# Kernel tuning notes

Measured on AMD Instinct MI355X. Metric: run time of the kernel, lower is better.

Reference implementation:

```python
import jax, jax.numpy as jnp
import numpy as np

EPS = 1e-8  # torch F.cosine_similarity eps


def setup_inputs() -> dict:
    key = jax.random.key(0)
    ks = jax.random.split(key, 12)
    B, H, W, D, Tq = 16, 32, 32, 768, 1024
    s = 1.0 / np.sqrt(D)
    inp = {
        "image_features": jax.random.normal(ks[0], (B, H, W, D), jnp.float32),
        "text_features": jax.random.normal(ks[1], (B, Tq, D), jnp.float32),
        "image_padding_mask": jax.random.randint(ks[2], (B, H, W), 0, 2).astype(bool),
        "Wq": jax.random.normal(ks[3], (D, D), jnp.float32) * s,
        "bq": jnp.zeros((D,), jnp.float32),
        "Wk": jax.random.normal(ks[4], (D, D), jnp.float32) * s,
        "bk": jnp.zeros((D,), jnp.float32),
        "W1": jax.random.normal(ks[5], (16, 1), jnp.float32),
        "b1": jnp.zeros((16,), jnp.float32),
        "W2": jax.random.normal(ks[6], (1, 16), jnp.float32) * 0.25,
        "b2": jnp.zeros((1,), jnp.float32),
    }
    return inp


def reference(image_features, text_features, image_padding_mask,
              Wq, bq, Wk, bk, W1, b1, W2, b2):
    B, H, W_, D = image_features.shape
    # projections (torch Linear: x @ W.T + b)
    q = text_features @ Wq.T + bq                      # [B, Tq, D]
    k = (image_features @ Wk.T + bk).reshape(B, H * W_, D)  # [B, Tk, D]
    pad = image_padding_mask.reshape(B, H * W_)        # [B, Tk] True = pad
    # cosine similarity: normalize with eps-clamped norms, then dot
    qn = q / jnp.maximum(jnp.linalg.norm(q, axis=-1, keepdims=True), EPS)
    kn = k / jnp.maximum(jnp.linalg.norm(k, axis=-1, keepdims=True), EPS)
    scores = jnp.einsum('bqd,bkd->bqk', qn, kn)        # [B, Tq, Tk]
    scores = jnp.where(pad[:, None, :], -jnp.inf, scores)
    max_w = scores.max(axis=-1)                        # [B, Tq]
    # tiny MLP 1 -> 16 -> 1 with sigmoid
    h = jax.nn.relu(max_w[..., None] @ W1.T + b1)      # [B, Tq, 16]
    out = jax.nn.sigmoid(h @ W2.T + b2)[..., 0]        # [B, Tq]
    return out
```

## Files before the change

kernel.cpp:

```cpp
#include <hip/hip_runtime.h>
#include <math.h>

typedef float  f32x4 __attribute__((ext_vector_type(4)));
typedef short  s16x8 __attribute__((ext_vector_type(8)));
typedef unsigned short u16x4 __attribute__((ext_vector_type(4)));
typedef unsigned short u16x8 __attribute__((ext_vector_type(8)));

__device__ __forceinline__ unsigned short f2bf(float f) {
  unsigned u = __float_as_uint(f);
  u += 0x7FFFu + ((u >> 16) & 1u);
  return (unsigned short)(u >> 16);
}
__device__ __forceinline__ float bf2f(unsigned short h) {
  return __uint_as_float(((unsigned)h) << 16);
}
__device__ __forceinline__ unsigned fenc(float f) {
  unsigned u = __float_as_uint(f);
  return (u & 0x80000000u) ? ~u : (u | 0x80000000u);
}
__device__ __forceinline__ float fdec(unsigned u) {
  u = (u & 0x80000000u) ? (u & 0x7FFFFFFFu) : ~u;
  return __uint_as_float(u);
}
__device__ __forceinline__ void gload16(const void* g, void* l) {
  __builtin_amdgcn_global_load_lds(
      (const __attribute__((address_space(1))) unsigned int*)g,
      (__attribute__((address_space(3))) unsigned int*)l, 16, 0, 0);
}

__global__ __launch_bounds__(256) void init_bufs(unsigned* __restrict__ um,
                                                 float* __restrict__ qs,
                                                 float* __restrict__ ks, int n) {
  int i = blockIdx.x * 256 + threadIdx.x;
  if (i < n) { um[i] = 0x007FFFFFu; qs[i] = 0.f; ks[i] = 0.f; }
}

__global__ __launch_bounds__(256) void cvt2(const float* __restrict__ a,
                                            const float* __restrict__ b,
                                            unsigned short* __restrict__ da,
                                            unsigned short* __restrict__ db, int n4) {
  int i = blockIdx.x * 256 + threadIdx.x;
  int stride = gridDim.x * 256;
  for (; i < 2 * n4; i += stride) {
    const float* s = (i < n4) ? a : b;
    unsigned short* d = (i < n4) ? da : db;
    int j = (i < n4) ? i : i - n4;
    f32x4 v = ((const f32x4*)s)[j];
    u16x4 o;
    o[0] = f2bf(v[0]); o[1] = f2bf(v[1]); o[2] = f2bf(v[2]); o[3] = f2bf(v[3]);
    ((u16x4*)d)[j] = o;
  }
}

__global__ __launch_bounds__(256) void proj(const float* __restrict__ Xq,
                                            const float* __restrict__ Xk,
                                            const unsigned short* __restrict__ Wqb,
                                            const unsigned short* __restrict__ Wkb,
                                            const float* __restrict__ bq,
                                            const float* __restrict__ bk,
                                            unsigned short* __restrict__ Qh,
                                            unsigned short* __restrict__ Kh,
                                            float* __restrict__ qssq,
                                            float* __restrict__ kssq) {
  const int K = 768;
  __shared__ __align__(16) unsigned short sA[128 * 64];
  __shared__ __align__(16) unsigned short sB[128 * 64];
  int id = blockIdx.x;
  int xcd = id & 7, j = id >> 3;
  int by = j % 6, bxl = j / 6;
  int bx = xcd * 16 + bxl;
  const float* A; const unsigned short* Bw; const float* bias;
  unsigned short* Out; float* ssq;
  if (blockIdx.z == 0) { A = Xq; Bw = Wqb; bias = bq; Out = Qh; ssq = qssq; }
  else                 { A = Xk; Bw = Wkb; bias = bk; Out = Kh; ssq = kssq; }

  const int t = threadIdx.x;
  const int lane = t & 63, w = t >> 6;
  const int wr = w >> 1, wc = w & 1;
  const int m0 = bx * 128, n0 = by * 128;
  const float* Ab = A + (size_t)m0 * K;
  const unsigned short* Bb = Bw + (size_t)n0 * K;
  f32x4 acc[4][4] = {};
  const int srow = t >> 3;
  const int scol = (t & 7) * 8;
  const int hsw = scol ^ ((srow & 7) << 3);
  const int lg = lane >> 4, li = lane & 15;

  for (int k0 = 0; k0 < K; k0 += 64) {
#pragma unroll
    for (int s = 0; s < 4; ++s) {
      int row = srow + s * 32;
      gload16(Bb + (size_t)row * K + k0 + hsw, (char*)sB + t * 16 + s * 4096);
    }
#pragma unroll
    for (int s = 0; s < 4; ++s) {
      int row = srow + s * 32;
      const float* src = Ab + (size_t)row * K + k0 + scol;
      f32x4 v0 = *(const f32x4*)(src);
      f32x4 v1 = *(const f32x4*)(src + 4);
      u16x8 o;
      o[0] = f2bf(v0[0]); o[1] = f2bf(v0[1]); o[2] = f2bf(v0[2]); o[3] = f2bf(v0[3]);
      o[4] = f2bf(v1[0]); o[5] = f2bf(v1[1]); o[6] = f2bf(v1[2]); o[7] = f2bf(v1[3]);
      *(u16x8*)(sA + row * 64 + (scol ^ ((row & 7) << 3))) = o;
    }
    __syncthreads();
#pragma unroll
    for (int ks = 0; ks < 2; ++ks) {
      s16x8 af[4], bfr[4];
#pragma unroll
      for (int mi = 0; mi < 4; ++mi) {
        int row = wr * 64 + mi * 16 + li;
        af[mi] = *(const s16x8*)(sA + row * 64 + ((ks * 32 + lg * 8) ^ ((row & 7) << 3)));
      }
#pragma unroll
      for (int ni = 0; ni < 4; ++ni) {
        int row = wc * 64 + ni * 16 + li;
        bfr[ni] = *(const s16x8*)(sB + row * 64 + ((ks * 32 + lg * 8) ^ ((row & 7) << 3)));
      }
#pragma unroll
      for (int mi = 0; mi < 4; ++mi)
#pragma unroll
        for (int ni = 0; ni < 4; ++ni)
          acc[mi][ni] = __builtin_amdgcn_mfma_f32_16x16x32_bf16(af[mi], bfr[ni], acc[mi][ni], 0, 0, 0);
    }
    __syncthreads();
  }
  float bv[4]; int col[4];
#pragma unroll
  for (int ni = 0; ni < 4; ++ni) { col[ni] = n0 + wc * 64 + ni * 16 + li; bv[ni] = bias[col[ni]]; }
#pragma unroll
  for (int mi = 0; mi < 4; ++mi) {
    int rbase = m0 + wr * 64 + mi * 16 + lg * 4;
#pragma unroll
    for (int r = 0; r < 4; ++r) {
      float s = 0.f;
#pragma unroll
      for (int ni = 0; ni < 4; ++ni) {
        float v = acc[mi][ni][r] + bv[ni];
        Out[(size_t)(rbase + r) * 768 + col[ni]] = f2bf(v);
        s += v * v;
      }
#pragma unroll
      for (int off = 1; off < 16; off <<= 1) s += __shfl_xor(s, off, 64);
      if (li == 0) atomicAdd(&ssq[rbase + r], s);
    }
  }
}

__global__ __launch_bounds__(256) void scores_max(const unsigned short* __restrict__ Qh,
                                                  const unsigned short* __restrict__ Kh,
                                                  const float* __restrict__ kssq,
                                                  const int* __restrict__ pad,
                                                  unsigned* __restrict__ umax) {
  const int K = 768;
  __shared__ __align__(16) unsigned short sA[128 * 64];
  __shared__ __align__(16) unsigned short sB[128 * 64];
  int id = blockIdx.x;
  int x = id & 7, g = id >> 3;
  int tile = g & 63;
  int qt = tile & 7, kt = tile >> 3;
  int b = ((g >> 6) << 3) | x;

  const int t = threadIdx.x;
  const int lane = t & 63, w = t >> 6;
  const int wr = w >> 1, wc = w & 1;
  const unsigned short* Ab = Qh + ((size_t)b * 1024 + qt * 128) * K;
  const unsigned short* Bb = Kh + ((size_t)b * 1024 + kt * 128) * K;
  f32x4 acc[4][4] = {};
  const int srow = t >> 3;
  const int scol = (t & 7) * 8;
  const int hsw = scol ^ ((srow & 7) << 3);
  const int lg = lane >> 4, li = lane & 15;

  for (int k0 = 0; k0 < K; k0 += 64) {
#pragma unroll
    for (int s = 0; s < 4; ++s) {
      int row = srow + s * 32;
      gload16(Ab + (size_t)row * K + k0 + hsw, (char*)sA + t * 16 + s * 4096);
      gload16(Bb + (size_t)row * K + k0 + hsw, (char*)sB + t * 16 + s * 4096);
    }
    __syncthreads();
#pragma unroll
    for (int ks = 0; ks < 2; ++ks) {
      s16x8 af[4], bfr[4];
#pragma unroll
      for (int mi = 0; mi < 4; ++mi) {
        int row = wr * 64 + mi * 16 + li;
        af[mi] = *(const s16x8*)(sA + row * 64 + ((ks * 32 + lg * 8) ^ ((row & 7) << 3)));
      }
#pragma unroll
      for (int ni = 0; ni < 4; ++ni) {
        int row = wc * 64 + ni * 16 + li;
        bfr[ni] = *(const s16x8*)(sB + row * 64 + ((ks * 32 + lg * 8) ^ ((row & 7) << 3)));
      }
#pragma unroll
      for (int mi = 0; mi < 4; ++mi)
#pragma unroll
        for (int ni = 0; ni < 4; ++ni)
          acc[mi][ni] = __builtin_amdgcn_mfma_f32_16x16x32_bf16(af[mi], bfr[ni], acc[mi][ni], 0, 0, 0);
    }
    __syncthreads();
  }
  float rk[4]; bool valid[4];
#pragma unroll
  for (int ni = 0; ni < 4; ++ni) {
    int gcol = b * 1024 + kt * 128 + wc * 64 + ni * 16 + li;
    rk[ni] = 1.0f / fmaxf(sqrtf(kssq[gcol]), 1e-8f);
    valid[ni] = (pad[gcol] == 0);
  }
#pragma unroll
  for (int mi = 0; mi < 4; ++mi) {
#pragma unroll
    for (int r = 0; r < 4; ++r) {
      float v = -INFINITY;
#pragma unroll
      for (int ni = 0; ni < 4; ++ni)
        if (valid[ni]) v = fmaxf(v, acc[mi][ni][r] * rk[ni]);
#pragma unroll
      for (int off = 1; off < 16; off <<= 1) v = fmaxf(v, __shfl_xor(v, off, 64));
      if (li == 0) {
        int row = b * 1024 + qt * 128 + wr * 64 + mi * 16 + lg * 4 + r;
        atomicMax(&umax[row], fenc(v));
      }
    }
  }
}

__global__ __launch_bounds__(256) void mlp_kernel(const unsigned* __restrict__ umax,
                                                  const float* __restrict__ qssq,
                                                  const float* __restrict__ w1,
                                                  const float* __restrict__ b1,
                                                  const float* __restrict__ w2,
                                                  const float* __restrict__ b2,
                                                  float* __restrict__ out, int n) {
  int i = blockIdx.x * 256 + threadIdx.x;
  if (i >= n) return;
  float m = fdec(umax[i]) / fmaxf(sqrtf(qssq[i]), 1e-8f);
  float s = b2[0];
#pragma unroll
  for (int j = 0; j < 16; ++j) s += w2[j] * fmaxf(m * w1[j] + b1[j], 0.f);
  out[i] = 1.f / (1.f + expf(-s));
}

extern "C" void kernel_launch(void* const* d_in, const int* in_sizes, int n_in,
                              void* d_out, int out_size, void* d_ws, size_t ws_size,
                              hipStream_t stream) {
  const float* image = (const float*)d_in[0];
  const float* text  = (const float*)d_in[1];
  const int*   pad   = (const int*)d_in[2];
  const float* Wq    = (const float*)d_in[3];
  const float* bq    = (const float*)d_in[4];
  const float* Wk    = (const float*)d_in[5];
  const float* bk    = (const float*)d_in[6];
  const float* W1    = (const float*)d_in[7];
  const float* b1    = (const float*)d_in[8];
  const float* W2    = (const float*)d_in[9];
  const float* b2    = (const float*)d_in[10];
  float* out = (float*)d_out;

  char* ws = (char*)d_ws;
  unsigned short* Qh  = (unsigned short*)(ws);
  unsigned short* Kh  = (unsigned short*)(ws + 25165824);
  unsigned short* Wqb = (unsigned short*)(ws + 50331648);
  unsigned short* Wkb = (unsigned short*)(ws + 51511296);
  unsigned*       um  = (unsigned*)(ws + 52690944);
  float*          qss = (float*)(ws + 52756480);
  float*          kss = (float*)(ws + 52822016);

  init_bufs<<<64, 256, 0, stream>>>(um, qss, kss, 16384);
  cvt2<<<1152, 256, 0, stream>>>(Wq, Wk, Wqb, Wkb, 147456);
  proj<<<dim3(768, 1, 2), 256, 0, stream>>>(text, image, Wqb, Wkb, bq, bk, Qh, Kh, qss, kss);
  scores_max<<<1024, 256, 0, stream>>>(Qh, Kh, kss, pad, um);
  mlp_kernel<<<64, 256, 0, stream>>>(um, qss, W1, b1, W2, b2, out, 16384);
}
```

Before: 243.7 us.

## Double-buffer LDS in both GEMMs and fuse MLP epilogue via tile ticket counter

Both the projection GEMM and the scores GEMM now use two LDS buffers, prefetching the next K-slice while MFMAs run on the current one, which removes one barrier per iteration. The init kernel is replaced by a memset, using a shifted max encoding so that zero is the identity. The separate MLP kernel is folded into scores_max: the last block to finish each query tile (found with an atomic ticket counter) applies the MLP. This cuts two launches and hides load latency, at the cost of doubled LDS (64KB per block), which may lower occupancy.

```diff
diff --git a/kernel.cpp b/kernel.cpp
--- a/kernel.cpp
+++ b/kernel.cpp
@@ -11,14 +11,13 @@
   u += 0x7FFFu + ((u >> 16) & 1u);
   return (unsigned short)(u >> 16);
 }
-__device__ __forceinline__ float bf2f(unsigned short h) {
-  return __uint_as_float(((unsigned)h) << 16);
-}
-__device__ __forceinline__ unsigned fenc(float f) {
+__device__ __forceinline__ unsigned fenc2(float f) {
   unsigned u = __float_as_uint(f);
-  return (u & 0x80000000u) ? ~u : (u | 0x80000000u);
-}
-__device__ __forceinline__ float fdec(unsigned u) {
+  u = (u & 0x80000000u) ? ~u : (u | 0x80000000u);
+  return u - 0x007FFFFFu;
+}
+__device__ __forceinline__ float fdec2(unsigned u) {
+  u += 0x007FFFFFu;
   u = (u & 0x80000000u) ? (u & 0x7FFFFFFFu) : ~u;
   return __uint_as_float(u);
 }
@@ -26,13 +25,6 @@
   __builtin_amdgcn_global_load_lds(
       (const __attribute__((address_space(1))) unsigned int*)g,
       (__attribute__((address_space(3))) unsigned int*)l, 16, 0, 0);
-}
-
-__global__ __launch_bounds__(256) void init_bufs(unsigned* __restrict__ um,
-                                                 float* __restrict__ qs,
-                                                 float* __restrict__ ks, int n) {
-  int i = blockIdx.x * 256 + threadIdx.x;
-  if (i < n) { um[i] = 0x007FFFFFu; qs[i] = 0.f; ks[i] = 0.f; }
 }
 
 __global__ __launch_bounds__(256) void cvt2(const float* __restrict__ a,
@@ -63,8 +55,8 @@
                                             float* __restrict__ qssq,
                                             float* __restrict__ kssq) {
   const int K = 768;
-  __shared__ __align__(16) unsigned short sA[128 * 64];
-  __shared__ __align__(16) unsigned short sB[128 * 64];
+  __shared__ __align__(16) unsigned short sA[2][128 * 64];
+  __shared__ __align__(16) unsigned short sB[2][128 * 64];
   int id = blockIdx.x;
   int xcd = id & 7, j = id >> 3;
   int by = j % 6, bxl = j / 6;
@@ -86,42 +78,76 @@
   const int hsw = scol ^ ((srow & 7) << 3);
   const int lg = lane >> 4, li = lane & 15;
 
-  for (int k0 = 0; k0 < K; k0 += 64) {
+#pragma unroll
+  for (int s = 0; s < 4; ++s) {
+    int row = srow + s * 32;
+    gload16(Bb + (size_t)row * K + hsw, (char*)sB[0] + t * 16 + s * 4096);
+  }
+  {
+    f32x4 v0[4], v1[4];
+#pragma unroll
+    for (int s = 0; s < 4; ++s) {
+      const float* src = Ab + (size_t)(srow + s * 32) * K + scol;
+      v0[s] = *(const f32x4*)src; v1[s] = *(const f32x4*)(src + 4);
+    }
 #pragma unroll
     for (int s = 0; s < 4; ++s) {
       int row = srow + s * 32;
-      gload16(Bb + (size_t)row * K + k0 + hsw, (char*)sB + t * 16 + s * 4096);
-    }
-#pragma unroll
-    for (int s = 0; s < 4; ++s) {
-      int row = srow + s * 32;
-      const float* src = Ab + (size_t)row * K + k0 + scol;
-      f32x4 v0 = *(const f32x4*)(src);
-      f32x4 v1 = *(const f32x4*)(src + 4);
       u16x8 o;
-      o[0] = f2bf(v0[0]); o[1] = f2bf(v0[1]); o[2] = f2bf(v0[2]); o[3] = f2bf(v0[3]);
-      o[4] = f2bf(v1[0]); o[5] = f2bf(v1[1]); o[6] = f2bf(v1[2]); o[7] = f2bf(v1[3]);
-      *(u16x8*)(sA + row * 64 + (scol ^ ((row & 7) << 3))) = o;
-    }
-    __syncthreads();
+      o[0] = f2bf(v0[s][0]); o[1] = f2bf(v0[s][1]); o[2] = f2bf(v0[s][2]); o[3] = f2bf(v0[s][3]);
+      o[4] = f2bf(v1[s][0]); o[5] = f2bf(v1[s][1]); o[6] = f2bf(v1[s][2]); o[7] = f2bf(v1[s][3]);
+      *(u16x8*)(sA[0] + row * 64 + (scol ^ ((row & 7) << 3))) = o;
+    }
+  }
+  __syncthreads();
+
+  for (int kt = 0; kt < 12; ++kt) {
+    const int cur = kt & 1;
+    const unsigned short* cA = sA[cur];
+    const unsigned short* cB = sB[cur];
+    f32x4 p0[4], p1[4];
+    const bool pre = (kt < 11);
+    if (pre) {
+      const int k0n = (kt + 1) * 64;
+#pragma unroll
+      for (int s = 0; s < 4; ++s) {
+        int row = srow + s * 32;
+        gload16(Bb + (size_t)row * K + k0n + hsw, (char*)sB[cur ^ 1] + t * 16 + s * 4096);
+      }
+#pragma unroll
+      for (int s = 0; s < 4; ++s) {
+        const float* src = Ab + (size_t)(srow + s * 32) * K + k0n + scol;
+        p0[s] = *(const f32x4*)src; p1[s] = *(const f32x4*)(src + 4);
+      }
+    }
 #pragma unroll
     for (int ks = 0; ks < 2; ++ks) {
       s16x8 af[4], bfr[4];
 #pragma unroll
       for (int mi = 0; mi < 4; ++mi) {
         int row = wr * 64 + mi * 16 + li;
-        af[mi] = *(const s16x8*)(sA + row * 64 + ((ks * 32 + lg * 8) ^ ((row & 7) << 3)));
+        af[mi] = *(const s16x8*)(cA + row * 64 + ((ks * 32 + lg * 8) ^ ((row & 7) << 3)));
       }
 #pragma unroll
       for (int ni = 0; ni < 4; ++ni) {
         int row = wc * 64 + ni * 16 + li;
-        bfr[ni] = *(const s16x8*)(sB + row * 64 + ((ks * 32 + lg * 8) ^ ((row & 7) << 3)));
+        bfr[ni] = *(const s16x8*)(cB + row * 64 + ((ks * 32 + lg * 8) ^ ((row & 7) << 3)));
       }
 #pragma unroll
       for (int mi = 0; mi < 4; ++mi)
 #pragma unroll
         for (int ni = 0; ni < 4; ++ni)
           acc[mi][ni] = __builtin_amdgcn_mfma_f32_16x16x32_bf16(af[mi], bfr[ni], acc[mi][ni], 0, 0, 0);
+    }
+    if (pre) {
+#pragma unroll
+      for (int s = 0; s < 4; ++s) {
+        int row = srow + s * 32;
+        u16x8 o;
+        o[0] = f2bf(p0[s][0]); o[1] = f2bf(p0[s][1]); o[2] = f2bf(p0[s][2]); o[3] = f2bf(p0[s][3]);
+        o[4] = f2bf(p1[s][0]); o[5] = f2bf(p1[s][1]); o[6] = f2bf(p1[s][2]); o[7] = f2bf(p1[s][3]);
+        *(u16x8*)(sA[cur ^ 1] + row * 64 + (scol ^ ((row & 7) << 3))) = o;
+      }
     }
     __syncthreads();
   }
@@ -150,48 +176,69 @@
 __global__ __launch_bounds__(256) void scores_max(const unsigned short* __restrict__ Qh,
                                                   const unsigned short* __restrict__ Kh,
                                                   const float* __restrict__ kssq,
+                                                  const float* __restrict__ qssq,
                                                   const int* __restrict__ pad,
-                                                  unsigned* __restrict__ umax) {
+                                                  const float* __restrict__ w1,
+                                                  const float* __restrict__ b1,
+                                                  const float* __restrict__ w2,
+                                                  const float* __restrict__ b2,
+                                                  unsigned* __restrict__ umax,
+                                                  unsigned* __restrict__ cnt,
+                                                  float* __restrict__ out) {
   const int K = 768;
-  __shared__ __align__(16) unsigned short sA[128 * 64];
-  __shared__ __align__(16) unsigned short sB[128 * 64];
+  __shared__ __align__(16) unsigned short sA[2][128 * 64];
+  __shared__ __align__(16) unsigned short sB[2][128 * 64];
+  __shared__ int sTicket;
   int id = blockIdx.x;
   int x = id & 7, g = id >> 3;
   int tile = g & 63;
-  int qt = tile & 7, kt = tile >> 3;
+  int qt = tile & 7, kt_ = tile >> 3;
   int b = ((g >> 6) << 3) | x;
 
   const int t = threadIdx.x;
   const int lane = t & 63, w = t >> 6;
   const int wr = w >> 1, wc = w & 1;
   const unsigned short* Ab = Qh + ((size_t)b * 1024 + qt * 128) * K;
-  const unsigned short* Bb = Kh + ((size_t)b * 1024 + kt * 128) * K;
+  const unsigned short* Bb = Kh + ((size_t)b * 1024 + kt_ * 128) * K;
   f32x4 acc[4][4] = {};
   const int srow = t >> 3;
   const int scol = (t & 7) * 8;
   const int hsw = scol ^ ((srow & 7) << 3);
   const int lg = lane >> 4, li = lane & 15;
 
-  for (int k0 = 0; k0 < K; k0 += 64) {
-#pragma unroll
-    for (int s = 0; s < 4; ++s) {
-      int row = srow + s * 32;
-      gload16(Ab + (size_t)row * K + k0 + hsw, (char*)sA + t * 16 + s * 4096);
-      gload16(Bb + (size_t)row * K + k0 + hsw, (char*)sB + t * 16 + s * 4096);
-    }
-    __syncthreads();
+#pragma unroll
+  for (int s = 0; s < 4; ++s) {
+    int row = srow + s * 32;
+    gload16(Ab + (size_t)row * K + hsw, (char*)sA[0] + t * 16 + s * 4096);
+    gload16(Bb + (size_t)row * K + hsw, (char*)sB[0] + t * 16 + s * 4096);
+  }
+  __syncthreads();
+
+  for (int kt = 0; kt < 12; ++kt) {
+    const int cur = kt & 1;
+    const unsigned short* cA = sA[cur];
+    const unsigned short* cB = sB[cur];
+    if (kt < 11) {
+      const int k0n = (kt + 1) * 64;
+#pragma unroll
+      for (int s = 0; s < 4; ++s) {
+        int row = srow + s * 32;
+        gload16(Ab + (size_t)row * K + k0n + hsw, (char*)sA[cur ^ 1] + t * 16 + s * 4096);
+        gload16(Bb + (size_t)row * K + k0n + hsw, (char*)sB[cur ^ 1] + t * 16 + s * 4096);
+      }
+    }
 #pragma unroll
     for (int ks = 0; ks < 2; ++ks) {
       s16x8 af[4], bfr[4];
 #pragma unroll
       for (int mi = 0; mi < 4; ++mi) {
         int row = wr * 64 + mi * 16 + li;
-        af[mi] = *(const s16x8*)(sA + row * 64 + ((ks * 32 + lg * 8) ^ ((row & 7) << 3)));
+        af[mi] = *(const s16x8*)(cA + row * 64 + ((ks * 32 + lg * 8) ^ ((row & 7) << 3)));
       }
 #pragma unroll
       for (int ni = 0; ni < 4; ++ni) {
         int row = wc * 64 + ni * 16 + li;
-        bfr[ni] = *(const s16x8*)(sB + row * 64 + ((ks * 32 + lg * 8) ^ ((row & 7) << 3)));
+        bfr[ni] = *(const s16x8*)(cB + row * 64 + ((ks * 32 + lg * 8) ^ ((row & 7) << 3)));
       }
 #pragma unroll
       for (int mi = 0; mi < 4; ++mi)
@@ -204,7 +251,7 @@
   float rk[4]; bool valid[4];
 #pragma unroll
   for (int ni = 0; ni < 4; ++ni) {
-    int gcol = b * 1024 + kt * 128 + wc * 64 + ni * 16 + li;
+    int gcol = b * 1024 + kt_ * 128 + wc * 64 + ni * 16 + li;
     rk[ni] = 1.0f / fmaxf(sqrtf(kssq[gcol]), 1e-8f);
     valid[ni] = (pad[gcol] == 0);
   }
@@ -220,26 +267,27 @@
       for (int off = 1; off < 16; off <<= 1) v = fmaxf(v, __shfl_xor(v, off, 64));
       if (li == 0) {
         int row = b * 1024 + qt * 128 + wr * 64 + mi * 16 + lg * 4 + r;
-        atomicMax(&umax[row], fenc(v));
-      }
-    }
-  }
-}
-
-__global__ __launch_bounds__(256) void mlp_kernel(const unsigned* __restrict__ umax,
-                                                  const float* __restrict__ qssq,
-                                                  const float* __restrict__ w1,
-                                                  const float* __restrict__ b1,
-                                                  const float* __restrict__ w2,
-                                                  const float* __restrict__ b2,
-                                                  float* __restrict__ out, int n) {
-  int i = blockIdx.x * 256 + threadIdx.x;
-  if (i >= n) return;
-  float m = fdec(umax[i]) / fmaxf(sqrtf(qssq[i]), 1e-8f);
-  float s = b2[0];
-#pragma unroll
-  for (int j = 0; j < 16; ++j) s += w2[j] * fmaxf(m * w1[j] + b1[j], 0.f);
-  out[i] = 1.f / (1.f + expf(-s));
+        unsigned e = fenc2(v);
+        if (e) atomicMax(&umax[row], e);
+      }
+    }
+  }
+  __threadfence();
+  __syncthreads();
+  if (t == 0) sTicket = (int)atomicAdd(&cnt[b * 8 + qt], 1u);
+  __syncthreads();
+  if (sTicket == 7) {
+    __threadfence();
+    if (t < 128) {
+      int row = b * 1024 + qt * 128 + t;
+      unsigned u = atomicAdd(&umax[row], 0u);
+      float m = fdec2(u) / fmaxf(sqrtf(qssq[row]), 1e-8f);
+      float s = b2[0];
+#pragma unroll
+      for (int jj = 0; jj < 16; ++jj) s += w2[jj] * fmaxf(m * w1[jj] + b1[jj], 0.f);
+      out[row] = 1.f / (1.f + expf(-s));
+    }
+  }
 }
 
 extern "C" void kernel_launch(void* const* d_in, const int* in_sizes, int n_in,
@@ -259,17 +307,17 @@
   float* out = (float*)d_out;
 
   char* ws = (char*)d_ws;
-  unsigned short* Qh  = (unsigned short*)(ws);
-  unsigned short* Kh  = (unsigned short*)(ws + 25165824);
-  unsigned short* Wqb = (unsigned short*)(ws + 50331648);
-  unsigned short* Wkb = (unsigned short*)(ws + 51511296);
-  unsigned*       um  = (unsigned*)(ws + 52690944);
-  float*          qss = (float*)(ws + 52756480);
-  float*          kss = (float*)(ws + 52822016);
-
-  init_bufs<<<64, 256, 0, stream>>>(um, qss, kss, 16384);
+  unsigned*       um  = (unsigned*)(ws);
+  float*          qss = (float*)(ws + 65536);
+  float*          kss = (float*)(ws + 131072);
+  unsigned*       cnt = (unsigned*)(ws + 196608);
+  unsigned short* Qh  = (unsigned short*)(ws + 262144);
+  unsigned short* Kh  = (unsigned short*)(ws + 262144 + 25165824);
+  unsigned short* Wqb = (unsigned short*)(ws + 262144 + 50331648);
+  unsigned short* Wkb = (unsigned short*)(ws + 262144 + 51511296);
+
+  hipMemsetAsync(ws, 0, 262144, stream);
   cvt2<<<1152, 256, 0, stream>>>(Wq, Wk, Wqb, Wkb, 147456);
   proj<<<dim3(768, 1, 2), 256, 0, stream>>>(text, image, Wqb, Wkb, bq, bk, Qh, Kh, qss, kss);
-  scores_max<<<1024, 256, 0, stream>>>(Qh, Kh, kss, pad, um);
-  mlp_kernel<<<64, 256, 0, stream>>>(um, qss, W1, b1, W2, b2, out, 16384);
-}
+  scores_max<<<1024, 256, 0, stream>>>(Qh, Kh, kss, qss, pad, W1, b1, W2, b2, um, cnt, out);
+}
```

Result: slower. 326.8 us (+34.1%).

## Pre-convert activations to bf16 and split projection into two async-load GEMMs

Applied to the files above, without the earlier changes.

Text and image activations are now converted to bf16 in separate elementwise passes, one reusing a shared scratch buffer. The projection GEMM can then load A through global_load_lds as well, instead of converting fp32 to bf16 inside the GEMM loop. Buffer initialisation is folded into the conversion kernel through an offset encoding that lets zero serve as the identity for max, and atomics for encoded zero are skipped. This adds two extra full read/write passes over the activations and serialises the Q and K projections, each now launched with half the previous total block count.

```diff
diff --git a/kernel.cpp b/kernel.cpp
--- a/kernel.cpp
+++ b/kernel.cpp
@@ -4,21 +4,19 @@
 typedef float  f32x4 __attribute__((ext_vector_type(4)));
 typedef short  s16x8 __attribute__((ext_vector_type(8)));
 typedef unsigned short u16x4 __attribute__((ext_vector_type(4)));
-typedef unsigned short u16x8 __attribute__((ext_vector_type(8)));
 
 __device__ __forceinline__ unsigned short f2bf(float f) {
   unsigned u = __float_as_uint(f);
   u += 0x7FFFu + ((u >> 16) & 1u);
   return (unsigned short)(u >> 16);
 }
-__device__ __forceinline__ float bf2f(unsigned short h) {
-  return __uint_as_float(((unsigned)h) << 16);
-}
-__device__ __forceinline__ unsigned fenc(float f) {
+__device__ __forceinline__ unsigned fenc2(float f) {
   unsigned u = __float_as_uint(f);
-  return (u & 0x80000000u) ? ~u : (u | 0x80000000u);
-}
-__device__ __forceinline__ float fdec(unsigned u) {
+  u = (u & 0x80000000u) ? ~u : (u | 0x80000000u);
+  return u - 0x007FFFFFu;
+}
+__device__ __forceinline__ float fdec2(unsigned u) {
+  u += 0x007FFFFFu;
   u = (u & 0x80000000u) ? (u & 0x7FFFFFFFu) : ~u;
   return __uint_as_float(u);
 }
@@ -28,23 +26,23 @@
       (__attribute__((address_space(3))) unsigned int*)l, 16, 0, 0);
 }
 
-__global__ __launch_bounds__(256) void init_bufs(unsigned* __restrict__ um,
-                                                 float* __restrict__ qs,
-                                                 float* __restrict__ ks, int n) {
-  int i = blockIdx.x * 256 + threadIdx.x;
-  if (i < n) { um[i] = 0x007FFFFFu; qs[i] = 0.f; ks[i] = 0.f; }
-}
-
-__global__ __launch_bounds__(256) void cvt2(const float* __restrict__ a,
-                                            const float* __restrict__ b,
-                                            unsigned short* __restrict__ da,
-                                            unsigned short* __restrict__ db, int n4) {
-  int i = blockIdx.x * 256 + threadIdx.x;
-  int stride = gridDim.x * 256;
-  for (; i < 2 * n4; i += stride) {
-    const float* s = (i < n4) ? a : b;
-    unsigned short* d = (i < n4) ? da : db;
-    int j = (i < n4) ? i : i - n4;
+__global__ __launch_bounds__(256) void cvt_prep(const float* __restrict__ Wq,
+                                                const float* __restrict__ Wk,
+                                                const float* __restrict__ text,
+                                                unsigned short* __restrict__ Wqb,
+                                                unsigned short* __restrict__ Wkb,
+                                                unsigned short* __restrict__ Xb,
+                                                unsigned* __restrict__ initzone) {
+  const int NW = 147456;
+  const int NT = 3145728;
+  int tid = blockIdx.x * 256 + threadIdx.x;
+  int nth = gridDim.x * 256;
+  if (tid < 49152) initzone[tid] = 0;
+  for (int i = tid; i < 2 * NW + NT; i += nth) {
+    const float* s; unsigned short* d; int j;
+    if (i < NW)            { s = Wq;   d = Wqb; j = i; }
+    else if (i < 2 * NW)   { s = Wk;   d = Wkb; j = i - NW; }
+    else                   { s = text; d = Xb;  j = i - 2 * NW; }
     f32x4 v = ((const f32x4*)s)[j];
     u16x4 o;
     o[0] = f2bf(v[0]); o[1] = f2bf(v[1]); o[2] = f2bf(v[2]); o[3] = f2bf(v[3]);
@@ -52,16 +50,23 @@
   }
 }
 
-__global__ __launch_bounds__(256) void proj(const float* __restrict__ Xq,
-                                            const float* __restrict__ Xk,
-                                            const unsigned short* __restrict__ Wqb,
-                                            const unsigned short* __restrict__ Wkb,
-                                            const float* __restrict__ bq,
-                                            const float* __restrict__ bk,
-                                            unsigned short* __restrict__ Qh,
-                                            unsigned short* __restrict__ Kh,
-                                            float* __restrict__ qssq,
-                                            float* __restrict__ kssq) {
+__global__ __launch_bounds__(256) void cvt_one(const float* __restrict__ src,
+                                               unsigned short* __restrict__ dst, int n4) {
+  int i = blockIdx.x * 256 + threadIdx.x;
+  int stride = gridDim.x * 256;
+  for (; i < n4; i += stride) {
+    f32x4 v = ((const f32x4*)src)[i];
+    u16x4 o;
+    o[0] = f2bf(v[0]); o[1] = f2bf(v[1]); o[2] = f2bf(v[2]); o[3] = f2bf(v[3]);
+    ((u16x4*)dst)[i] = o;
+  }
+}
+
+__global__ __launch_bounds__(256) void projv2(const unsigned short* __restrict__ A,
+                                              const unsigned short* __restrict__ Bw,
+                                              const float* __restrict__ bias,
+                                              unsigned short* __restrict__ Out,
+                                              float* __restrict__ ssq) {
   const int K = 768;
   __shared__ __align__(16) unsigned short sA[128 * 64];
   __shared__ __align__(16) unsigned short sB[128 * 64];
@@ -69,16 +74,12 @@
   int xcd = id & 7, j = id >> 3;
   int by = j % 6, bxl = j / 6;
   int bx = xcd * 16 + bxl;
-  const float* A; const unsigned short* Bw; const float* bias;
-  unsigned short* Out; float* ssq;
-  if (blockIdx.z == 0) { A = Xq; Bw = Wqb; bias = bq; Out = Qh; ssq = qssq; }
-  else                 { A = Xk; Bw = Wkb; bias = bk; Out = Kh; ssq = kssq; }
 
   const int t = threadIdx.x;
   const int lane = t & 63, w = t >> 6;
   const int wr = w >> 1, wc = w & 1;
   const int m0 = bx * 128, n0 = by * 128;
-  const float* Ab = A + (size_t)m0 * K;
+  const unsigned short* Ab = A + (size_t)m0 * K;
   const unsigned short* Bb = Bw + (size_t)n0 * K;
   f32x4 acc[4][4] = {};
   const int srow = t >> 3;
@@ -90,18 +91,8 @@
 #pragma unroll
     for (int s = 0; s < 4; ++s) {
       int row = srow + s * 32;
+      gload16(Ab + (size_t)row * K + k0 + hsw, (char*)sA + t * 16 + s * 4096);
       gload16(Bb + (size_t)row * K + k0 + hsw, (char*)sB + t * 16 + s * 4096);
-    }
-#pragma unroll
-    for (int s = 0; s < 4; ++s) {
-      int row = srow + s * 32;
-      const float* src = Ab + (size_t)row * K + k0 + scol;
-      f32x4 v0 = *(const f32x4*)(src);
-      f32x4 v1 = *(const f32x4*)(src + 4);
-      u16x8 o;
-      o[0] = f2bf(v0[0]); o[1] = f2bf(v0[1]); o[2] = f2bf(v0[2]); o[3] = f2bf(v0[3]);
-      o[4] = f2bf(v1[0]); o[5] = f2bf(v1[1]); o[6] = f2bf(v1[2]); o[7] = f2bf(v1[3]);
-      *(u16x8*)(sA + row * 64 + (scol ^ ((row & 7) << 3))) = o;
     }
     __syncthreads();
 #pragma unroll
@@ -158,14 +149,14 @@
   int id = blockIdx.x;
   int x = id & 7, g = id >> 3;
   int tile = g & 63;
-  int qt = tile & 7, kt = tile >> 3;
+  int qt = tile & 7, kt_ = tile >> 3;
   int b = ((g >> 6) << 3) | x;
 
   const int t = threadIdx.x;
   const int lane = t & 63, w = t >> 6;
   const int wr = w >> 1, wc = w & 1;
   const unsigned short* Ab = Qh + ((size_t)b * 1024 + qt * 128) * K;
-  const unsigned short* Bb = Kh + ((size_t)b * 1024 + kt * 128) * K;
+  const unsigned short* Bb = Kh + ((size_t)b * 1024 + kt_ * 128) * K;
   f32x4 acc[4][4] = {};
   const int srow = t >> 3;
   const int scol = (t & 7) * 8;
@@ -204,7 +195,7 @@
   float rk[4]; bool valid[4];
 #pragma unroll
   for (int ni = 0; ni < 4; ++ni) {
-    int gcol = b * 1024 + kt * 128 + wc * 64 + ni * 16 + li;
+    int gcol = b * 1024 + kt_ * 128 + wc * 64 + ni * 16 + li;
     rk[ni] = 1.0f / fmaxf(sqrtf(kssq[gcol]), 1e-8f);
     valid[ni] = (pad[gcol] == 0);
   }
@@ -220,7 +211,8 @@
       for (int off = 1; off < 16; off <<= 1) v = fmaxf(v, __shfl_xor(v, off, 64));
       if (li == 0) {
         int row = b * 1024 + qt * 128 + wr * 64 + mi * 16 + lg * 4 + r;
-        atomicMax(&umax[row], fenc(v));
+        unsigned e = fenc2(v);
+        if (e) atomicMax(&umax[row], e);
       }
     }
   }
@@ -235,7 +227,7 @@
                                                   float* __restrict__ out, int n) {
   int i = blockIdx.x * 256 + threadIdx.x;
   if (i >= n) return;
-  float m = fdec(umax[i]) / fmaxf(sqrtf(qssq[i]), 1e-8f);
+  float m = fdec2(umax[i]) / fmaxf(sqrtf(qssq[i]), 1e-8f);
   float s = b2[0];
 #pragma unroll
   for (int j = 0; j < 16; ++j) s += w2[j] * fmaxf(m * w1[j] + b1[j], 0.f);
@@ -259,17 +251,19 @@
   float* out = (float*)d_out;
 
   char* ws = (char*)d_ws;
-  unsigned short* Qh  = (unsigned short*)(ws);
-  unsigned short* Kh  = (unsigned short*)(ws + 25165824);
-  unsigned short* Wqb = (unsigned short*)(ws + 50331648);
-  unsigned short* Wkb = (unsigned short*)(ws + 51511296);
-  unsigned*       um  = (unsigned*)(ws + 52690944);
-  float*          qss = (float*)(ws + 52756480);
-  float*          kss = (float*)(ws + 52822016);
-
-  init_bufs<<<64, 256, 0, stream>>>(um, qss, kss, 16384);
-  cvt2<<<1152, 256, 0, stream>>>(Wq, Wk, Wqb, Wkb, 147456);
-  proj<<<dim3(768, 1, 2), 256, 0, stream>>>(text, image, Wqb, Wkb, bq, bk, Qh, Kh, qss, kss);
+  unsigned*       um  = (unsigned*)(ws);
+  float*          qss = (float*)(ws + 65536);
+  float*          kss = (float*)(ws + 131072);
+  unsigned short* Wqb = (unsigned short*)(ws + 196608);
+  unsigned short* Wkb = (unsigned short*)(ws + 1376256);
+  unsigned short* Qh  = (unsigned short*)(ws + 2555904);
+  unsigned short* Kh  = (unsigned short*)(ws + 27721728);
+  unsigned short* Xb  = (unsigned short*)(ws + 52887552);
+
+  cvt_prep<<<2048, 256, 0, stream>>>(Wq, Wk, text, Wqb, Wkb, Xb, um);
+  projv2<<<768, 256, 0, stream>>>(Xb, Wqb, bq, Qh, qss);
+  cvt_one<<<2048, 256, 0, stream>>>(image, Xb, 3145728);
+  projv2<<<768, 256, 0, stream>>>(Xb, Wkb, bk, Kh, kss);
   scores_max<<<1024, 256, 0, stream>>>(Qh, Kh, kss, pad, um);
   mlp_kernel<<<64, 256, 0, stream>>>(um, qss, W1, b1, W2, b2, out, 16384);
 }
```

Result: slower. 259.1 us (+6.3%).
